# Kernel tuning notes

Hardware: AMD Instinct MI355X
Metric: run time of the kernel (lower is better)

## Reference

```python
import jax, jax.numpy as jnp
import numpy as np

EPS = 1e-5
TEMPERATURE = 0.07

def _layernorm(x, g, b):
    m = jnp.mean(x, axis=-1, keepdims=True)
    v = jnp.mean(jnp.square(x - m), axis=-1, keepdims=True)
    return (x - m) * jax.lax.rsqrt(v + EPS) * g + b

def _proj(x, W, b, g, beta):
    # Linear -> LayerNorm -> ReLU (Dropout is identity in eval)
    return jax.nn.relu(_layernorm(x @ W + b, g, beta))

def setup_inputs() -> dict:
    key = jax.random.key(0)
    B, S, Dv, Dl, D = 8, 2048, 768, 768, 768
    ks = jax.random.split(key, 8)
    def lin(k, din, dout):
        return jax.random.normal(k, (din, dout), jnp.float32) / np.sqrt(din)
    return {
        "vision_features": jax.random.normal(ks[0], (B, S, Dv), jnp.float32),
        "language_features": jax.random.normal(ks[1], (B, S, Dl), jnp.float32),
        "vW": lin(ks[2], Dv, D), "vb": jnp.zeros((D,), jnp.float32),
        "vg": jnp.ones((D,), jnp.float32), "vbeta": jnp.zeros((D,), jnp.float32),
        "lW": lin(ks[3], Dl, D), "lb": jnp.zeros((D,), jnp.float32),
        "lg": jnp.ones((D,), jnp.float32), "lbeta": jnp.zeros((D,), jnp.float32),
        "claw": lin(ks[4], D, D),  # claw_matrix parameter [D, D]
        "oW": lin(ks[5], 2 * D, D), "ob": jnp.zeros((D,), jnp.float32),
        "og": jnp.ones((D,), jnp.float32), "obeta": jnp.zeros((D,), jnp.float32),
    }

def reference(vision_features, language_features, vW, vb, vg, vbeta,
              lW, lb, lg, lbeta, claw, oW, ob, og, obeta):
    vp = _proj(vision_features, vW, vb, vg, vbeta)      # [B,S,D]
    lp = _proj(language_features, lW, lb, lg, lbeta)    # [B,S,D]
    # similarity / temperature, scaled by mean of learned claw matrix
    sim = jnp.einsum('bsd,btd->bst', vp, lp) * (claw.mean() / TEMPERATURE)
    A = jax.nn.softmax(sim, axis=-1)                    # [B,S,S] claw matrix
    aligned_vision = jnp.einsum('bst,btd->bsd', A, vp)  # A @ vp
    aligned_language = jnp.einsum('bst,bsd->btd', A, lp)  # A^T @ lp
    combined = jnp.concatenate([aligned_vision, aligned_language], axis=-1)
    return jax.nn.relu(_layernorm(combined @ oW + ob, og, obeta))
```

## Files before the change

### kernel.cpp

```cpp
#include <hip/hip_runtime.h>
#include <hip/hip_bf16.h>

typedef short short8 __attribute__((ext_vector_type(8)));
typedef float f32x4 __attribute__((ext_vector_type(4)));
typedef unsigned short u16;

#define BK 32
static __device__ __forceinline__ int sw(int row, int g) {
  return row * 32 + ((g ^ ((row >> 3) & 3)) << 3);
}

static __device__ __forceinline__ u16 f2b(float f) {
  union { float f; unsigned u; } x; x.f = f;
  unsigned r = x.u + 0x7FFF + ((x.u >> 16) & 1);
  return (u16)(r >> 16);
}
static __device__ __forceinline__ float b2f(u16 u) {
  unsigned int x = ((unsigned int)u) << 16;
  float f; __builtin_memcpy(&f, &x, 4);
  return f;
}

static __device__ __forceinline__ void load8(const u16* p, u16* dst) {
  union { uint4 u; u16 h[8]; } t;
  t.u = *(const uint4*)p;
  #pragma unroll
  for (int j = 0; j < 8; ++j) dst[j] = t.h[j];
}
static __device__ __forceinline__ void load8(const float* p, u16* dst) {
  float4 a = ((const float4*)p)[0];
  float4 b = ((const float4*)p)[1];
  dst[0] = f2b(a.x); dst[1] = f2b(a.y); dst[2] = f2b(a.z); dst[3] = f2b(a.w);
  dst[4] = f2b(b.x); dst[5] = f2b(b.y); dst[6] = f2b(b.z); dst[7] = f2b(b.w);
}

static __device__ __forceinline__ void gl_lds16(const u16* g, u16* l) {
  __builtin_amdgcn_global_load_lds(
      (const __attribute__((address_space(1))) unsigned int*)g,
      (__attribute__((address_space(3))) unsigned int*)l, 16, 0, 0);
}

template<int MA, int MB, typename OutT>
__global__ __launch_bounds__(256) void gemm128(
    const u16* __restrict__ A, const u16* __restrict__ B,
    const float* __restrict__ bias, const float* __restrict__ alpha_ptr,
    OutT* __restrict__ C, int K, int lda, int ldb, int ldc,
    long long sA, long long sB, long long sC)
{
  __shared__ u16 As[128 * 32];
  __shared__ u16 Bs[128 * 32];

  A += (long long)blockIdx.z * sA;
  B += (long long)blockIdx.z * sB;
  C += (long long)blockIdx.z * sC;

  const int tid  = threadIdx.x;
  const int m0   = blockIdx.y * 128;
  const int n0   = blockIdx.x * 128;
  const int w    = tid >> 6, lane = tid & 63;
  const int wm   = (w >> 1) * 64;
  const int wn   = (w & 1) * 64;
  const int lrow = lane & 15;
  const int lg   = lane >> 4;

  int aoff[4], boff[4];
  #pragma unroll
  for (int t = 0; t < 4; ++t) {
    const int ar = wm + t * 16 + lrow;
    const int br = wn + t * 16 + lrow;
    aoff[t] = (MA == 1) ? sw(ar, lg) : ar * 32 + lg * 8;
    boff[t] = (MB == 1) ? sw(br, lg) : br * 32 + lg * 8;
  }

  f32x4 acc[4][4] = {};

  for (int k0 = 0; k0 < K; k0 += BK) {
    if constexpr (MA == 0) {
      gl_lds16(A + (long long)(m0 + (tid >> 2)) * lda + (k0 + (tid & 3) * 8),
               As + tid * 8);
      gl_lds16(A + (long long)(m0 + 64 + (tid >> 2)) * lda + (k0 + (tid & 3) * 8),
               As + 2048 + tid * 8);
    } else {
      const int kk = tid >> 3;
      #pragma unroll
      for (int p = 0; p < 2; ++p) {
        const int rr = (tid & 7) * 8 + p * 64;
        u16 h[8];
        load8(A + (long long)(k0 + kk) * lda + (m0 + rr), h);
        #pragma unroll
        for (int j = 0; j < 8; ++j) As[sw(rr + j, kk >> 3) + (kk & 7)] = h[j];
      }
    }
    if constexpr (MB == 0) {
      gl_lds16(B + (long long)(n0 + (tid >> 2)) * ldb + (k0 + (tid & 3) * 8),
               Bs + tid * 8);
      gl_lds16(B + (long long)(n0 + 64 + (tid >> 2)) * ldb + (k0 + (tid & 3) * 8),
               Bs + 2048 + tid * 8);
    } else {
      const int kk = tid >> 3;
      #pragma unroll
      for (int p = 0; p < 2; ++p) {
        const int rr = (tid & 7) * 8 + p * 64;
        u16 h[8];
        load8(B + (long long)(k0 + kk) * ldb + (n0 + rr), h);
        #pragma unroll
        for (int j = 0; j < 8; ++j) Bs[sw(rr + j, kk >> 3) + (kk & 7)] = h[j];
      }
    }
    __syncthreads();

    short8 af[4], bf[4];
    #pragma unroll
    for (int t = 0; t < 4; ++t) af[t] = *(const short8*)(As + aoff[t]);
    #pragma unroll
    for (int t = 0; t < 4; ++t) bf[t] = *(const short8*)(Bs + boff[t]);
    #pragma unroll
    for (int mt = 0; mt < 4; ++mt)
      #pragma unroll
      for (int nt = 0; nt < 4; ++nt)
        acc[mt][nt] = __builtin_amdgcn_mfma_f32_16x16x32_bf16(
            af[mt], bf[nt], acc[mt][nt], 0, 0, 0);
    __syncthreads();
  }

  const float alpha = alpha_ptr ? *alpha_ptr : 1.0f;
  #pragma unroll
  for (int nt = 0; nt < 4; ++nt) {
    const int n = n0 + wn + nt * 16 + lrow;
    const float bv = bias ? bias[n] : 0.0f;
    #pragma unroll
    for (int mt = 0; mt < 4; ++mt) {
      #pragma unroll
      for (int r = 0; r < 4; ++r) {
        const int m = m0 + wm + mt * 16 + lg * 4 + r;
        C[(long long)m * ldc + n] = OutT(acc[mt][nt][r] * alpha + bv);
      }
    }
  }
}

template<typename T>
__global__ __launch_bounds__(256) void transpose_kernel(
    const T* __restrict__ in, u16* __restrict__ out, int R, int C,
    long long sIn, long long sOut)
{
  __shared__ u16 t[64][66];
  in  += (long long)blockIdx.z * sIn;
  out += (long long)blockIdx.z * sOut;
  const int r0 = blockIdx.y * 64, c0 = blockIdx.x * 64;
  const int tid = threadIdx.x;
  const int rr = tid >> 3, cc = (tid & 7) * 8;
  #pragma unroll
  for (int p = 0; p < 2; ++p) {
    union { uint4 u; unsigned w[4]; u16 h[8]; } v;
    const int row = rr + p * 32;
    load8(in + (long long)(r0 + row) * C + (c0 + cc), v.h);
    #pragma unroll
    for (int k = 0; k < 4; ++k)
      *(unsigned*)&t[row][cc + k * 2] = v.w[k];
  }
  __syncthreads();
  #pragma unroll
  for (int p = 0; p < 2; ++p) {
    const int oc = (tid >> 3) + p * 32;
    const int rc = (tid & 7) * 8;
    union { uint4 u; u16 h[8]; } g;
    #pragma unroll
    for (int j = 0; j < 8; ++j) g.h[j] = t[rc + j][oc];
    *(uint4*)(out + (long long)(c0 + oc) * R + (r0 + rc)) = g.u;
  }
}

__global__ __launch_bounds__(256) void cvt_kernel(
    const float* __restrict__ in, u16* __restrict__ out, int n8)
{
  const int stride = gridDim.x * 256;
  for (int i = blockIdx.x * 256 + threadIdx.x; i < n8; i += stride) {
    union { uint4 u; u16 h[8]; } v;
    load8(in + (long long)i * 8, v.h);
    *(uint4*)(out + (long long)i * 8) = v.u;
  }
}

template<typename OutT>
__global__ __launch_bounds__(256) void ln_relu_kernel(
    const float* __restrict__ x, const float* __restrict__ g,
    const float* __restrict__ beta, OutT* __restrict__ out)
{
  __shared__ float sa[4], sb[4];
  const float* xr = x + (long long)blockIdx.x * 768;
  float v[3]; float s = 0.f, ss = 0.f;
  #pragma unroll
  for (int j = 0; j < 3; ++j) {
    v[j] = xr[threadIdx.x + j * 256];
    s += v[j]; ss += v[j] * v[j];
  }
  #pragma unroll
  for (int off = 32; off; off >>= 1) {
    s  += __shfl_down(s, off);
    ss += __shfl_down(ss, off);
  }
  const int w = threadIdx.x >> 6, lane = threadIdx.x & 63;
  if (!lane) { sa[w] = s; sb[w] = ss; }
  __syncthreads();
  s  = sa[0] + sa[1] + sa[2] + sa[3];
  ss = sb[0] + sb[1] + sb[2] + sb[3];
  const float mean = s * (1.f / 768.f);
  const float var  = ss * (1.f / 768.f) - mean * mean;
  const float rst  = rsqrtf(var + 1e-5f);
  OutT* orow = out + (long long)blockIdx.x * 768;
  #pragma unroll
  for (int j = 0; j < 3; ++j) {
    const int idx = threadIdx.x + j * 256;
    const float yv = (v[j] - mean) * rst * g[idx] + beta[idx];
    const float rv = (yv <= 0.f) ? 0.f : yv;
    orow[idx] = OutT(rv);
  }
}

__global__ __launch_bounds__(256) void softmax_kernel(u16* __restrict__ sim)
{
  __shared__ float sm[4], ssum[4];
  u16* row = sim + (long long)blockIdx.x * 2048;
  union { uint4 u; u16 h[8]; } v;
  v.u = *(const uint4*)(row + threadIdx.x * 8);
  float f[8]; float mx = -1e30f;
  #pragma unroll
  for (int j = 0; j < 8; ++j) { f[j] = b2f(v.h[j]); mx = fmaxf(mx, f[j]); }
  #pragma unroll
  for (int off = 32; off; off >>= 1) mx = fmaxf(mx, __shfl_down(mx, off));
  const int w = threadIdx.x >> 6, lane = threadIdx.x & 63;
  if (!lane) sm[w] = mx;
  __syncthreads();
  mx = fmaxf(fmaxf(sm[0], sm[1]), fmaxf(sm[2], sm[3]));
  float s = 0.f;
  #pragma unroll
  for (int j = 0; j < 8; ++j) { f[j] = __expf(f[j] - mx); s += f[j]; }
  #pragma unroll
  for (int off = 32; off; off >>= 1) s += __shfl_down(s, off);
  if (!lane) ssum[w] = s;
  __syncthreads();
  s = ssum[0] + ssum[1] + ssum[2] + ssum[3];
  const float inv = 1.f / s;
  #pragma unroll
  for (int j = 0; j < 8; ++j) v.h[j] = f2b(f[j] * inv);
  *(uint4*)(row + threadIdx.x * 8) = v.u;
}

__global__ __launch_bounds__(256) void claw_partial_kernel(
    const float* __restrict__ claw, float* __restrict__ partial, int n)
{
  __shared__ float sa[4];
  float s = 0.f;
  const int nv = n >> 2;
  for (int i = blockIdx.x * 256 + threadIdx.x; i < nv; i += 64 * 256) {
    float4 v = ((const float4*)claw)[i];
    s += v.x + v.y + v.z + v.w;
  }
  #pragma unroll
  for (int off = 32; off; off >>= 1) s += __shfl_down(s, off);
  const int w = threadIdx.x >> 6, lane = threadIdx.x & 63;
  if (!lane) sa[w] = s;
  __syncthreads();
  if (threadIdx.x == 0)
    partial[blockIdx.x] = sa[0] + sa[1] + sa[2] + sa[3];
}

__global__ void claw_final_kernel(
    const float* __restrict__ partial, float* __restrict__ scale, float inv)
{
  float s = partial[threadIdx.x];
  #pragma unroll
  for (int off = 32; off; off >>= 1) s += __shfl_down(s, off);
  if (threadIdx.x == 0) *scale = s * inv;
}

extern "C" void kernel_launch(void* const* d_in, const int* in_sizes, int n_in,
                              void* d_out, int out_size, void* d_ws, size_t ws_size,
                              hipStream_t stream)
{
  const float* vis   = (const float*)d_in[0];
  const float* lang  = (const float*)d_in[1];
  const float* vW    = (const float*)d_in[2];
  const float* vb    = (const float*)d_in[3];
  const float* vg    = (const float*)d_in[4];
  const float* vbeta = (const float*)d_in[5];
  const float* lW    = (const float*)d_in[6];
  const float* lb    = (const float*)d_in[7];
  const float* lg    = (const float*)d_in[8];
  const float* lbeta = (const float*)d_in[9];
  const float* claw  = (const float*)d_in[10];
  const float* oW    = (const float*)d_in[11];
  const float* ob    = (const float*)d_in[12];
  const float* og    = (const float*)d_in[13];
  const float* obeta = (const float*)d_in[14];
  float* out = (float*)d_out;

  constexpr int NB = 8, S = 2048, D = 768;
  constexpr int R = NB * S;
  constexpr long long SD = (long long)S * D;
  constexpr long long SS = (long long)S * S;
  const int nclaw = in_sizes[10];
  const float claw_inv = 1.0f / ((float)nclaw * 0.07f);
  const dim3 blk(256);

  char* ws = (char*)d_ws;
  u16*   vp    = (u16*)  (ws);
  u16*   lp    = (u16*)  (ws + 25165824);
  u16*   visb  = (u16*)  (ws + 50331648);
  u16*   vpT   = (u16*)  (ws + 50331648);
  u16*   langb = (u16*)  (ws + 75497472);
  u16*   lpT   = (u16*)  (ws + 75497472);
  u16*   sim   = (u16*)  (ws + 100663296);
  float* y     = (float*)(ws + 100663296);
  u16*   vWT   = (u16*)  (ws + 150994944);
  u16*   lWT   = vWT + 589824;
  u16*   oWT   = (u16*)  (ws + 150994944);
  u16*   comb  = (u16*)  (ws);
  float* scale   = (float*)(ws + 167772160);
  float* partial = (float*)(ws + 167772176);

  claw_partial_kernel<<<64, blk, 0, stream>>>(claw, partial, nclaw);
  claw_final_kernel<<<1, 64, 0, stream>>>(partial, scale, claw_inv);

  transpose_kernel<float><<<dim3(12, 12, 1), blk, 0, stream>>>(
      vW, vWT, D, D, 0, 0);
  transpose_kernel<float><<<dim3(12, 12, 1), blk, 0, stream>>>(
      lW, lWT, D, D, 0, 0);

  cvt_kernel<<<2048, blk, 0, stream>>>(vis, visb, (int)(R * D / 8));
  gemm128<0, 0, float><<<dim3(D / 128, R / 128, 1), blk, 0, stream>>>(
      visb, vWT, vb, nullptr, y, D, D, D, D, 0, 0, 0);
  ln_relu_kernel<__hip_bfloat16><<<R, blk, 0, stream>>>(
      y, vg, vbeta, (__hip_bfloat16*)vp);
  transpose_kernel<u16><<<dim3(D / 64, S / 64, NB), blk, 0, stream>>>(
      vp, vpT, S, D, SD, SD);

  cvt_kernel<<<2048, blk, 0, stream>>>(lang, langb, (int)(R * D / 8));
  gemm128<0, 0, float><<<dim3(D / 128, R / 128, 1), blk, 0, stream>>>(
      langb, lWT, lb, nullptr, y, D, D, D, D, 0, 0, 0);
  ln_relu_kernel<__hip_bfloat16><<<R, blk, 0, stream>>>(
      y, lg, lbeta, (__hip_bfloat16*)lp);
  transpose_kernel<u16><<<dim3(D / 64, S / 64, NB), blk, 0, stream>>>(
      lp, lpT, S, D, SD, SD);

  gemm128<0, 0, __hip_bfloat16><<<dim3(S / 128, S / 128, NB), blk, 0, stream>>>(
      vp, lp, nullptr, scale, (__hip_bfloat16*)sim, D, D, D, S, SD, SD, SS);
  softmax_kernel<<<R, blk, 0, stream>>>(sim);

  gemm128<0, 0, __hip_bfloat16><<<dim3(D / 128, S / 128, NB), blk, 0, stream>>>(
      sim, vpT, nullptr, nullptr, (__hip_bfloat16*)comb,
      S, S, S, 2 * D, SS, SD, 2 * SD);
  gemm128<1, 0, __hip_bfloat16><<<dim3(D / 128, S / 128, NB), blk, 0, stream>>>(
      sim, lpT, nullptr, nullptr, (__hip_bfloat16*)comb + D,
      S, S, S, 2 * D, SS, SD, 2 * SD);

  transpose_kernel<float><<<dim3(12, 24, 1), blk, 0, stream>>>(
      oW, oWT, 2 * D, D, 0, 0);

  gemm128<0, 0, float><<<dim3(D / 128, R / 128, 1), blk, 0, stream>>>(
      comb, oWT, ob, nullptr, y, 2 * D, 2 * D, 2 * D, D, 0, 0, 0);
  ln_relu_kernel<float><<<R, blk, 0, stream>>>(y, og, obeta, out);
}
```

Measured before the change: 645.4 us.

## Add 256x256 double-buffered GEMM kernel with interleaved loads and MFMA

```diff
diff --git a/kernel.cpp b/kernel.cpp
--- a/kernel.cpp
+++ b/kernel.cpp
@@ -38,6 +38,153 @@
   __builtin_amdgcn_global_load_lds(
       (const __attribute__((address_space(1))) unsigned int*)g,
       (__attribute__((address_space(3))) unsigned int*)l, 16, 0, 0);
+}
+
+template<typename OutT>
+__global__ __launch_bounds__(512, 2) void gemm256(
+    const u16* __restrict__ A, const u16* __restrict__ B,
+    const float* __restrict__ bias, const float* __restrict__ alpha_ptr,
+    OutT* __restrict__ C, int K, int lda, int ldb, int ldc,
+    long long sA, long long sB, long long sC)
+{
+  __shared__ u16 As[2][256 * 64];
+  __shared__ u16 Bs[2][256 * 64];
+
+  A += (long long)blockIdx.z * sA;
+  B += (long long)blockIdx.z * sB;
+  C += (long long)blockIdx.z * sC;
+
+  const int tid  = threadIdx.x;
+  const int m0   = blockIdx.y * 256;
+  const int n0   = blockIdx.x * 256;
+  const int w    = tid >> 6, lane = tid & 63;
+  const int wm   = (w >> 2) * 128;
+  const int wn   = (w & 3) * 64;
+  const int lrow = lane & 15;
+  const int lg   = lane >> 4;
+  const int xe   = ((lrow >> 2) & 1) << 1;
+  const int sr   = tid >> 3;
+  const int srcg = (tid & 7) ^ ((tid >> 4) & 2);
+  const int NT   = K >> 6;
+
+  f32x4 acc[8][4] = {};
+
+  auto stA = [&](int t, int c) {
+    u16* lb = As[t & 1];
+    const int r = (sr < 32) ? (32 * c + sr) : (96 + 32 * c + sr);
+    gl_lds16(A + (long long)(m0 + r) * lda + (t * 64 + srcg * 8),
+             lb + r * 64 + (tid & 7) * 8);
+  };
+  auto stB = [&](int t, int h) {
+    u16* lb = Bs[t & 1];
+    #pragma unroll
+    for (int l = 0; l < 2; ++l) {
+      const int r = 128 * h + 64 * l + sr;
+      gl_lds16(B + (long long)(n0 + r) * ldb + (t * 64 + srcg * 8),
+               lb + r * 64 + (tid & 7) * 8);
+    }
+  };
+  auto rdA = [&](int t, int mt, int ks) -> short8 {
+    const int r = wm + mt * 16 + lrow;
+    return *(const short8*)(As[t & 1] + r * 64 + (((ks * 4 + lg) ^ xe) << 3));
+  };
+  auto rdB = [&](int t, int nt, int ks) -> short8 {
+    const int r = wn + nt * 16 + lrow;
+    return *(const short8*)(Bs[t & 1] + r * 64 + (((ks * 4 + lg) ^ xe) << 3));
+  };
+
+  #pragma unroll
+  for (int c = 0; c < 4; ++c) stA(0, c);
+  stB(0, 0); stB(0, 1);
+  stA(1, 0); stA(1, 1); stA(1, 2);
+  asm volatile("s_waitcnt vmcnt(3)" ::: "memory");
+  __builtin_amdgcn_s_barrier();
+
+  short8 bfr[4][2];
+  for (int t = 0; t < NT; ++t) {
+    short8 afr[2][2];
+    #pragma unroll
+    for (int nt = 0; nt < 4; ++nt) {
+      bfr[nt][0] = rdB(t, nt, 0);
+      bfr[nt][1] = rdB(t, nt, 1);
+    }
+    afr[0][0] = rdA(t, 0, 0); afr[0][1] = rdA(t, 0, 1);
+    afr[1][0] = rdA(t, 1, 0); afr[1][1] = rdA(t, 1, 1);
+    if (t + 1 < NT) { stA(t + 1, 3); stB(t + 1, 0); }
+    __builtin_amdgcn_s_barrier();
+    __builtin_amdgcn_s_setprio(1);
+    #pragma unroll
+    for (int j = 0; j < 2; ++j)
+      #pragma unroll
+      for (int nt = 0; nt < 4; ++nt)
+        #pragma unroll
+        for (int ks = 0; ks < 2; ++ks)
+          acc[j][nt] = __builtin_amdgcn_mfma_f32_16x16x32_bf16(
+              afr[j][ks], bfr[nt][ks], acc[j][nt], 0, 0, 0);
+    __builtin_amdgcn_s_setprio(0);
+    __builtin_amdgcn_s_barrier();
+    afr[0][0] = rdA(t, 2, 0); afr[0][1] = rdA(t, 2, 1);
+    afr[1][0] = rdA(t, 3, 0); afr[1][1] = rdA(t, 3, 1);
+    if (t + 1 < NT) stB(t + 1, 1);
+    if (t + 2 < NT) stA(t + 2, 0);
+    __builtin_amdgcn_s_barrier();
+    __builtin_amdgcn_s_setprio(1);
+    #pragma unroll
+    for (int j = 0; j < 2; ++j)
+      #pragma unroll
+      for (int nt = 0; nt < 4; ++nt)
+        #pragma unroll
+        for (int ks = 0; ks < 2; ++ks)
+          acc[2 + j][nt] = __builtin_amdgcn_mfma_f32_16x16x32_bf16(
+              afr[j][ks], bfr[nt][ks], acc[2 + j][nt], 0, 0, 0);
+    __builtin_amdgcn_s_setprio(0);
+    __builtin_amdgcn_s_barrier();
+    afr[0][0] = rdA(t, 4, 0); afr[0][1] = rdA(t, 4, 1);
+    afr[1][0] = rdA(t, 5, 0); afr[1][1] = rdA(t, 5, 1);
+    if (t + 2 < NT) stA(t + 2, 1);
+    __builtin_amdgcn_s_barrier();
+    __builtin_amdgcn_s_setprio(1);
+    #pragma unroll
+    for (int j = 0; j < 2; ++j)
+      #pragma unroll
+      for (int nt = 0; nt < 4; ++nt)
+        #pragma unroll
+        for (int ks = 0; ks < 2; ++ks)
+          acc[4 + j][nt] = __builtin_amdgcn_mfma_f32_16x16x32_bf16(
+              afr[j][ks], bfr[nt][ks], acc[4 + j][nt], 0, 0, 0);
+    __builtin_amdgcn_s_setprio(0);
+    __builtin_amdgcn_s_barrier();
+    afr[0][0] = rdA(t, 6, 0); afr[0][1] = rdA(t, 6, 1);
+    afr[1][0] = rdA(t, 7, 0); afr[1][1] = rdA(t, 7, 1);
+    if (t + 2 < NT) stA(t + 2, 2);
+    __builtin_amdgcn_s_barrier();
+    __builtin_amdgcn_s_setprio(1);
+    #pragma unroll
+    for (int j = 0; j < 2; ++j)
+      #pragma unroll
+      for (int nt = 0; nt < 4; ++nt)
+        #pragma unroll
+        for (int ks = 0; ks < 2; ++ks)
+          acc[6 + j][nt] = __builtin_amdgcn_mfma_f32_16x16x32_bf16(
+              afr[j][ks], bfr[nt][ks], acc[6 + j][nt], 0, 0, 0);
+    __builtin_amdgcn_s_setprio(0);
+    asm volatile("s_waitcnt vmcnt(3)" ::: "memory");
+    __builtin_amdgcn_s_barrier();
+  }
+
+  const float alpha = alpha_ptr ? *alpha_ptr : 1.0f;
+  #pragma unroll
+  for (int nt = 0; nt < 4; ++nt) {
+    const int n = n0 + wn + nt * 16 + lrow;
+    const float bv = bias ? bias[n] : 0.0f;
+    #pragma unroll
+    for (int mt = 0; mt < 8; ++mt)
+      #pragma unroll
+      for (int r = 0; r < 4; ++r) {
+        const int m = m0 + wm + mt * 16 + lg * 4 + r;
+        C[(long long)m * ldc + n] = OutT(acc[mt][nt][r] * alpha + bv);
+      }
+  }
 }
 
 template<int MA, int MB, typename OutT>
@@ -303,6 +450,7 @@
   const int nclaw = in_sizes[10];
   const float claw_inv = 1.0f / ((float)nclaw * 0.07f);
   const dim3 blk(256);
+  const dim3 blk5(512);
 
   char* ws = (char*)d_ws;
   u16*   vp    = (u16*)  (ws);
@@ -329,7 +477,7 @@
       lW, lWT, D, D, 0, 0);
 
   cvt_kernel<<<2048, blk, 0, stream>>>(vis, visb, (int)(R * D / 8));
-  gemm128<0, 0, float><<<dim3(D / 128, R / 128, 1), blk, 0, stream>>>(
+  gemm256<float><<<dim3(D / 256, R / 256, 1), blk5, 0, stream>>>(
       visb, vWT, vb, nullptr, y, D, D, D, D, 0, 0, 0);
   ln_relu_kernel<__hip_bfloat16><<<R, blk, 0, stream>>>(
       y, vg, vbeta, (__hip_bfloat16*)vp);
@@ -337,18 +485,18 @@
       vp, vpT, S, D, SD, SD);
 
   cvt_kernel<<<2048, blk, 0, stream>>>(lang, langb, (int)(R * D / 8));
-  gemm128<0, 0, float><<<dim3(D / 128, R / 128, 1), blk, 0, stream>>>(
+  gemm256<float><<<dim3(D / 256, R / 256, 1), blk5, 0, stream>>>(
       langb, lWT, lb, nullptr, y, D, D, D, D, 0, 0, 0);
   ln_relu_kernel<__hip_bfloat16><<<R, blk, 0, stream>>>(
       y, lg, lbeta, (__hip_bfloat16*)lp);
   transpose_kernel<u16><<<dim3(D / 64, S / 64, NB), blk, 0, stream>>>(
       lp, lpT, S, D, SD, SD);
 
-  gemm128<0, 0, __hip_bfloat16><<<dim3(S / 128, S / 128, NB), blk, 0, stream>>>(
+  gemm256<__hip_bfloat16><<<dim3(S / 256, S / 256, NB), blk5, 0, stream>>>(
       vp, lp, nullptr, scale, (__hip_bfloat16*)sim, D, D, D, S, SD, SD, SS);
   softmax_kernel<<<R, blk, 0, stream>>>(sim);
 
-  gemm128<0, 0, __hip_bfloat16><<<dim3(D / 128, S / 128, NB), blk, 0, stream>>>(
+  gemm256<__hip_bfloat16><<<dim3(D / 256, S / 256, NB), blk5, 0, stream>>>(
       sim, vpT, nullptr, nullptr, (__hip_bfloat16*)comb,
       S, S, S, 2 * D, SS, SD, 2 * SD);
   gemm128<1, 0, __hip_bfloat16><<<dim3(D / 128, S / 128, NB), blk, 0, stream>>>(
@@ -358,7 +506,7 @@
   transpose_kernel<float><<<dim3(12, 24, 1), blk, 0, stream>>>(
       oW, oWT, 2 * D, D, 0, 0);
 
-  gemm128<0, 0, float><<<dim3(D / 128, R / 128, 1), blk, 0, stream>>>(
+  gemm256<float><<<dim3(D / 256, R / 256, 1), blk5, 0, stream>>>(
       comb, oWT, ob, nullptr, y, 2 * D, 2 * D, 2 * D, D, 0, 0, 0);
   ln_relu_kernel<float><<<R, blk, 0, stream>>>(y, og, obeta, out);
 }
```

Measured after the change: 625.7 us. 1.03x faster.
